# Kernel tuning notes

Hardware: AMD Instinct MI355X
Metric: run time of the kernel (lower is better)

## Reference

```python
import jax, jax.numpy as jnp
import numpy as np

N_NODES = 50000
N_EDGES = 800000
D = 128


def _degrees(idx, n):
    # in/out degree via segment_sum of ones, clamped to >=1 (DGL clamp)
    ones = jnp.ones(idx.shape[0], dtype=jnp.float32)
    return jnp.clip(jax.ops.segment_sum(ones, idx, num_segments=n), 1.0)


def graph_conv(x, src, dst, W, b):
    # DGL GraphConv, norm='both', aggregate-then-matmul (in_feats == out_feats)
    n = x.shape[0]
    deg_out = _degrees(src, n)  # [N]
    deg_in = _degrees(dst, n)   # [N]
    xs = x * jax.lax.rsqrt(deg_out)[:, None]          # [N, D] pre-normalize
    msg = jax.ops.segment_sum(xs[src], dst, num_segments=n)  # gather+scatter [N, D]
    h = msg * jax.lax.rsqrt(deg_in)[:, None]
    return h @ W + b


def setup_inputs() -> dict:
    key = jax.random.key(0)
    k1, k2, k3, k4, k5 = jax.random.split(key, 5)
    x = jax.random.normal(k1, (N_NODES, D), dtype=jnp.float32)
    src = jax.random.randint(k2, (N_EDGES,), 0, N_NODES, dtype=jnp.int64)
    dst = jax.random.randint(k3, (N_EDGES,), 0, N_NODES, dtype=jnp.int64)
    scale = 1.0 / np.sqrt(D)
    W1 = jax.random.normal(k4, (D, D), dtype=jnp.float32) * scale
    W2 = jax.random.normal(k5, (D, D), dtype=jnp.float32) * scale
    b1 = jnp.zeros((D,), dtype=jnp.float32)
    b2 = jnp.zeros((D,), dtype=jnp.float32)
    return {"x": x, "src": src, "dst": dst, "W1": W1, "b1": b1, "W2": W2, "b2": b2}


def reference(x, src, dst, W1, b1, W2, b2):
    h = graph_conv(x, src, dst, W1, b1)
    h = jax.nn.relu(h)
    return graph_conv(h, src, dst, W2, b2)
```

## Files before the change

### kernel.cpp

```cpp
#include <hip/hip_runtime.h>

#define N_NODES 50000
#define N_EDGES 800000
#define D 128
#define CAP 64
#define OVF_CAP 4096

#define HB 160
#define CHUNK ((N_EDGES + HB - 1) / HB)
#define NW (N_NODES / 4)

typedef unsigned short bf16_t;
typedef __attribute__((ext_vector_type(8))) short short8v;
typedef __attribute__((ext_vector_type(4))) float f32x4;

__device__ inline float bf2f(bf16_t u) {
    union { unsigned int i; float f; } v;
    v.i = ((unsigned int)u) << 16;
    return v.f;
}
__device__ inline bf16_t f2bf(float f) {
    union { float f; unsigned int i; } v;
    v.f = f;
    unsigned int u = v.i;
    unsigned int r = (u + 0x7FFFu + ((u >> 16) & 1u)) >> 16;
    return (bf16_t)r;
}
__device__ inline float u2f_lo(unsigned int u) {
    union { unsigned int i; float f; } x; x.i = u << 16; return x.f;
}
__device__ inline float u2f_hi(unsigned int u) {
    union { unsigned int i; float f; } x; x.i = u & 0xFFFF0000u; return x.f;
}


__global__ __launch_bounds__(1024) void hist_kernel(const int* __restrict__ src,
                                                    const int* __restrict__ dst,
                                                    unsigned int* __restrict__ Hs,
                                                    unsigned int* __restrict__ Hd, int nE) {
    __shared__ unsigned int hs[NW];
    __shared__ unsigned int hd[NW];
    for (int i = threadIdx.x; i < NW; i += 1024) { hs[i] = 0u; hd[i] = 0u; }
    __syncthreads();
    int e0 = blockIdx.x * CHUNK;
    int e1 = min(e0 + CHUNK, nE);
    for (int e = e0 + (int)threadIdx.x; e < e1; e += 1024) {
        int s = src[e];
        int d = dst[e];
        atomicAdd(&hs[s >> 2], 1u << (8 * (s & 3)));
        atomicAdd(&hd[d >> 2], 1u << (8 * (d & 3)));
    }
    __syncthreads();
    unsigned int* Hsb = Hs + (size_t)blockIdx.x * NW;
    unsigned int* Hdb = Hd + (size_t)blockIdx.x * NW;
    for (int i = threadIdx.x; i < NW; i += 1024) { Hsb[i] = hs[i]; Hdb[i] = hd[i]; }
}

__global__ void scan_kernel(const unsigned int* __restrict__ Hs,
                            const unsigned int* __restrict__ Hd,
                            unsigned int* __restrict__ OFF,
                            int* __restrict__ cnt_s, int* __restrict__ cnt_d) {
    int w = blockIdx.x * 256 + (int)threadIdx.x;
    if (w >= NW) return;
    if (blockIdx.y == 0) {
        unsigned int run = 0;
        for (int b = 0; b < HB; b++) {
            unsigned int v = Hd[(size_t)b * NW + w];
            OFF[(size_t)b * NW + w] = run;
            run += v;
        }
        int4 c;
        c.x = (int)(run & 0xFFu); c.y = (int)((run >> 8) & 0xFFu);
        c.z = (int)((run >> 16) & 0xFFu); c.w = (int)(run >> 24);
        ((int4*)cnt_d)[w] = c;
    } else {
        unsigned int run = 0;
        for (int b = 0; b < HB; b++) run += Hs[(size_t)b * NW + w];
        int4 c;
        c.x = (int)(run & 0xFFu); c.y = (int)((run >> 8) & 0xFFu);
        c.z = (int)((run >> 16) & 0xFFu); c.w = (int)(run >> 24);
        ((int4*)cnt_s)[w] = c;
    }
}

__global__ __launch_bounds__(1024) void place_kernel(const int* __restrict__ src,
                                                     const int* __restrict__ dst,
                                                     const unsigned int* __restrict__ OFF,
                                                     unsigned short* __restrict__ bucket,
                                                     int* __restrict__ ovf_cnt,
                                                     int2* __restrict__ ovf, int nE) {
    __shared__ unsigned int cur[NW];
    const unsigned int* OFFb = OFF + (size_t)blockIdx.x * NW;
    for (int i = threadIdx.x; i < NW; i += 1024) cur[i] = OFFb[i];
    __syncthreads();
    int e0 = blockIdx.x * CHUNK;
    int e1 = min(e0 + CHUNK, nE);
    for (int e = e0 + (int)threadIdx.x; e < e1; e += 1024) {
        int s = src[e];
        int d = dst[e];
        int sh = 8 * (d & 3);
        unsigned int old = atomicAdd(&cur[d >> 2], 1u << sh);
        unsigned int q = (old >> sh) & 0xFFu;
        if (q < CAP) {
            bucket[(size_t)d * CAP + q] = (unsigned short)s;
        } else {
            int o = atomicAdd(ovf_cnt, 1);
            if (o < OVF_CAP) ovf[o] = make_int2(d, s);
        }
    }
}

__global__ void prescale_kernel(const float4* __restrict__ x, const int* __restrict__ cnt_s,
                                const int* __restrict__ cnt_d,
                                float* __restrict__ rs_out, float* __restrict__ rs_in,
                                ushort4* __restrict__ xs4, int nN) {
    int node = blockIdx.x * 8 + (threadIdx.x >> 5);
    int c = threadIdx.x & 31;
    if (node >= nN) return;
    float rs_o = 0.0f;
    if (c == 0) {
        rs_o = rsqrtf(fmaxf((float)cnt_s[node], 1.0f));
        rs_out[node] = rs_o;
        rs_in[node] = rsqrtf(fmaxf((float)cnt_d[node], 1.0f));
    }
    rs_o = __shfl(rs_o, threadIdx.x & 32);
    float4 v = x[(size_t)node * 32 + c];
    ushort4 o;
    o.x = f2bf(v.x * rs_o);
    o.y = f2bf(v.y * rs_o);
    o.z = f2bf(v.z * rs_o);
    o.w = f2bf(v.w * rs_o);
    xs4[(size_t)node * 32 + c] = o;
}

__global__ void gather_kernel(const uint4* __restrict__ xs,
                              const int* __restrict__ cnt_d,
                              const unsigned short* __restrict__ bucket,
                              float4* __restrict__ msg4, int nN) {
    int node = blockIdx.x * 16 + ((int)threadIdx.x >> 4);
    int lane = threadIdx.x & 15;
    if (node >= nN) return;
    const unsigned short* bk = bucket + (size_t)node * CAP;
    int cnt = min(cnt_d[node], CAP);
    float a[8];
#pragma unroll
    for (int k = 0; k < 8; k++) a[k] = 0.f;
#define ACC8(v)                                              \
    a[0] += u2f_lo(v.x); a[1] += u2f_hi(v.x);                \
    a[2] += u2f_lo(v.y); a[3] += u2f_hi(v.y);                \
    a[4] += u2f_lo(v.z); a[5] += u2f_hi(v.z);                \
    a[6] += u2f_lo(v.w); a[7] += u2f_hi(v.w);
    int e = 0;
    for (; e + 3 < cnt; e += 4) {
        int s0 = bk[e], s1 = bk[e + 1], s2 = bk[e + 2], s3 = bk[e + 3];
        uint4 v0 = xs[(size_t)s0 * 16 + lane];
        uint4 v1 = xs[(size_t)s1 * 16 + lane];
        uint4 v2 = xs[(size_t)s2 * 16 + lane];
        uint4 v3 = xs[(size_t)s3 * 16 + lane];
        ACC8(v0) ACC8(v1) ACC8(v2) ACC8(v3)
    }
    for (; e < cnt; e++) {
        int s0 = bk[e];
        uint4 v0 = xs[(size_t)s0 * 16 + lane];
        ACC8(v0)
    }
#undef ACC8
    size_t o = (size_t)node * 32 + lane * 2;
    msg4[o]     = make_float4(a[0], a[1], a[2], a[3]);
    msg4[o + 1] = make_float4(a[4], a[5], a[6], a[7]);
}

__global__ void ovf_kernel(const int2* __restrict__ ovf, const int* __restrict__ ovf_cnt,
                           const ushort4* __restrict__ xs4, float* __restrict__ msg) {
    int n = min(*ovf_cnt, OVF_CAP);
    int lane = threadIdx.x & 31;
    for (int i = (int)(threadIdx.x >> 5); i < n; i += 8) {
        int2 ds = ovf[i];
        ushort4 v = xs4[(size_t)ds.y * 32 + lane];
        float* m = msg + (size_t)ds.x * D + lane * 4;
        atomicAdd(m + 0, bf2f(v.x));
        atomicAdd(m + 1, bf2f(v.y));
        atomicAdd(m + 2, bf2f(v.z));
        atomicAdd(m + 3, bf2f(v.w));
    }
}

__global__ void wsplit_kernel(const float* __restrict__ W1, bf16_t* __restrict__ Wf1,
                              const float* __restrict__ W2, bf16_t* __restrict__ Wf2) {
    const float* W = blockIdx.y ? W2 : W1;
    bf16_t* Wf = blockIdx.y ? Wf2 : Wf1;
    int flat = blockIdx.x * 256 + (int)threadIdx.x;
    int lane = flat & 63;
    int c = (flat >> 6) & 7;
    int ks = flat >> 9;
    int n = c * 16 + (lane & 15);
    int kb = ks * 32 + (lane >> 4) * 8;
#pragma unroll
    for (int j = 0; j < 8; j++) {
        float w = W[(size_t)(kb + j) * D + n];
        bf16_t hi = f2bf(w);
        bf16_t lo = f2bf(w - bf2f(hi));
        Wf[(size_t)flat * 8 + j] = hi;
        Wf[(size_t)(2048 + flat) * 8 + j] = lo;
    }
}

template <bool RELU_OUTSCALE, bool OUT_BF16>
__global__ __launch_bounds__(256) void gemm_mfma_kernel(
    const float* __restrict__ msg, const float* __restrict__ rs_in,
    const float* __restrict__ rs_out, const bf16_t* __restrict__ Wf,
    const float* __restrict__ bias, void* __restrict__ outp, int nN) {
    int lane = (int)threadIdx.x & 63;
    int wave = (int)threadIdx.x >> 6;
    int n0 = blockIdx.x * 64 + wave * 16;
    int ar = lane & 15;
    int kg = lane >> 4;

    short8v ahi[4], alo[4];
    {
        const float* ap = msg + (size_t)(n0 + ar) * D + kg * 8;
        bool valid = (n0 + ar) < nN;
#pragma unroll
        for (int ks = 0; ks < 4; ks++) {
            float av[8];
            if (valid) {
                float4 p0 = *(const float4*)(ap + ks * 32);
                float4 p1 = *(const float4*)(ap + ks * 32 + 4);
                av[0] = p0.x; av[1] = p0.y; av[2] = p0.z; av[3] = p0.w;
                av[4] = p1.x; av[5] = p1.y; av[6] = p1.z; av[7] = p1.w;
            } else {
#pragma unroll
                for (int j = 0; j < 8; j++) av[j] = 0.f;
            }
#pragma unroll
            for (int j = 0; j < 8; j++) {
                bf16_t h = f2bf(av[j]);
                bf16_t l = f2bf(av[j] - bf2f(h));
                ahi[ks][j] = (short)h;
                alo[ks][j] = (short)l;
            }
        }
    }

    f32x4 acc[8];
#pragma unroll
    for (int c = 0; c < 8; c++) acc[c] = (f32x4){0.f, 0.f, 0.f, 0.f};

    const short8v* Bh = (const short8v*)Wf;
    const short8v* Bl = Bh + 2048;
#pragma unroll
    for (int ks = 0; ks < 4; ks++) {
#pragma unroll
        for (int c = 0; c < 8; c++) {
            int off = (ks * 8 + c) * 64 + lane;
            short8v wh = Bh[off];
            short8v wl = Bl[off];
            acc[c] = __builtin_amdgcn_mfma_f32_16x16x32_bf16(ahi[ks], wh, acc[c], 0, 0, 0);
            acc[c] = __builtin_amdgcn_mfma_f32_16x16x32_bf16(alo[ks], wh, acc[c], 0, 0, 0);
            acc[c] = __builtin_amdgcn_mfma_f32_16x16x32_bf16(ahi[ks], wl, acc[c], 0, 0, 0);
        }
    }

    int ocol = lane & 15;
#pragma unroll
    for (int r = 0; r < 4; r++) {
        int node = n0 + kg * 4 + r;
        if (node >= nN) continue;
        float ri = rs_in[node];
        float ro = RELU_OUTSCALE ? rs_out[node] : 1.0f;
#pragma unroll
        for (int c = 0; c < 8; c++) {
            float v = acc[c][r] * ri + bias[c * 16 + ocol];
            if (RELU_OUTSCALE) v = fmaxf(v, 0.0f) * ro;
            if (OUT_BF16) {
                ((bf16_t*)outp)[(size_t)node * D + c * 16 + ocol] = f2bf(v);
            } else {
                ((float*)outp)[(size_t)node * D + c * 16 + ocol] = v;
            }
        }
    }
}

static inline size_t align16(size_t x) { return (x + 15) & ~(size_t)15; }

extern "C" void kernel_launch(void* const* d_in, const int* in_sizes, int n_in,
                              void* d_out, int out_size, void* d_ws, size_t ws_size,
                              hipStream_t stream) {
    const float* x   = (const float*)d_in[0];
    const int*   src = (const int*)d_in[1];
    const int*   dst = (const int*)d_in[2];
    const float* W1  = (const float*)d_in[3];
    const float* b1  = (const float*)d_in[4];
    const float* W2  = (const float*)d_in[5];
    const float* b2  = (const float*)d_in[6];
    float* out = (float*)d_out;

    char* p = (char*)d_ws;
    float*          msg     = (float*)p;          p += align16((size_t)N_NODES * D * sizeof(float));
    int*            cnt_s   = (int*)p;            p += align16(N_NODES * sizeof(int));
    int*            cnt_d   = (int*)p;            p += align16(N_NODES * sizeof(int));
    int*            ovf_cnt = (int*)p;            p += align16(16 * sizeof(int));
    int2*           ovf     = (int2*)p;           p += align16((size_t)OVF_CAP * sizeof(int2));
    unsigned short* bucket  = (unsigned short*)p; p += align16((size_t)N_NODES * CAP * sizeof(unsigned short));
    float*          rs_out  = (float*)p;          p += align16(N_NODES * sizeof(float));
    float*          rs_in   = (float*)p;          p += align16(N_NODES * sizeof(float));
    bf16_t*         Wf1     = (bf16_t*)p;         p += align16((size_t)2 * 2048 * 8 * sizeof(bf16_t));
    bf16_t*         Wf2     = (bf16_t*)p;         p += align16((size_t)2 * 2048 * 8 * sizeof(bf16_t));
    bf16_t*         xs      = (bf16_t*)p;
    bf16_t*         hs      = xs;

    unsigned int* Hs  = (unsigned int*)msg;
    unsigned int* Hd  = Hs + (size_t)HB * NW;
    unsigned int* OFF = Hd + (size_t)HB * NW;

    hipMemsetAsync(ovf_cnt, 0, 16 * sizeof(int), stream);

    wsplit_kernel<<<dim3(8, 2), 256, 0, stream>>>(W1, Wf1, W2, Wf2);

    hist_kernel<<<HB, 1024, 0, stream>>>(src, dst, Hs, Hd, N_EDGES);
    scan_kernel<<<dim3((NW + 255) / 256, 2), 256, 0, stream>>>(Hs, Hd, OFF, cnt_s, cnt_d);
    place_kernel<<<HB, 1024, 0, stream>>>(src, dst, OFF, bucket, ovf_cnt, ovf, N_EDGES);

    prescale_kernel<<<(N_NODES + 7) / 8, 256, 0, stream>>>((const float4*)x, cnt_s, cnt_d,
                                                           rs_out, rs_in, (ushort4*)xs, N_NODES);

    int ggrid = (N_NODES + 15) / 16;
    int mgrid = (N_NODES + 63) / 64;

    gather_kernel<<<ggrid, 256, 0, stream>>>((const uint4*)xs, cnt_d, bucket,
                                             (float4*)msg, N_NODES);
    ovf_kernel<<<1, 256, 0, stream>>>(ovf, ovf_cnt, (const ushort4*)xs, msg);

    gemm_mfma_kernel<true, true><<<mgrid, 256, 0, stream>>>(
        msg, rs_in, rs_out, Wf1, b1, hs, N_NODES);

    gather_kernel<<<ggrid, 256, 0, stream>>>((const uint4*)hs, cnt_d, bucket,
                                             (float4*)msg, N_NODES);
    ovf_kernel<<<1, 256, 0, stream>>>(ovf, ovf_cnt, (const ushort4*)hs, msg);

    gemm_mfma_kernel<false, false><<<mgrid, 256, 0, stream>>>(
        msg, rs_in, nullptr, Wf2, b2, out, N_NODES);
}
```

Before: 243.0 us.

## Replace histogram/scan/place pipeline with single node-partitioned LDS bucket scatter kernel

Replaces the three-kernel CSR build (per-chunk histograms, a scan over 160 histograms, then placement) with one kernel of 40 blocks. Each block owns 1250 destination nodes, reads the whole edge list, builds its buckets and degree counts in LDS, then writes them to global memory with coalesced stores. This removes the large intermediate histogram and offset traffic and two kernel launches. In exchange every block reads all 800K edges (40x redundant reads), only 40 CUs are used, and the per-node bucket capacity drops from 64 to 48, which may send more edges to the overflow path. Bucket slot order now depends on atomic timing rather than chunk order.

```diff
diff --git a/kernel.cpp b/kernel.cpp
--- a/kernel.cpp
+++ b/kernel.cpp
@@ -3,12 +3,11 @@
 #define N_NODES 50000
 #define N_EDGES 800000
 #define D 128
-#define CAP 64
+#define CAP 48
 #define OVF_CAP 4096
 
-#define HB 160
-#define CHUNK ((N_EDGES + HB - 1) / HB)
-#define NW (N_NODES / 4)
+#define NPART 40
+#define PNODES 1250
 
 typedef unsigned short bf16_t;
 typedef __attribute__((ext_vector_type(8))) short short8v;
@@ -33,80 +32,40 @@
     union { unsigned int i; float f; } x; x.i = u & 0xFFFF0000u; return x.f;
 }
 
-
-__global__ __launch_bounds__(1024) void hist_kernel(const int* __restrict__ src,
-                                                    const int* __restrict__ dst,
-                                                    unsigned int* __restrict__ Hs,
-                                                    unsigned int* __restrict__ Hd, int nE) {
-    __shared__ unsigned int hs[NW];
-    __shared__ unsigned int hd[NW];
-    for (int i = threadIdx.x; i < NW; i += 1024) { hs[i] = 0u; hd[i] = 0u; }
+__global__ __launch_bounds__(1024) void scatter_kernel(
+    const int* __restrict__ src, const int* __restrict__ dst,
+    unsigned short* __restrict__ bucket, int* __restrict__ cnt_s,
+    int* __restrict__ cnt_d, int* __restrict__ ovf_cnt, int2* __restrict__ ovf, int nE) {
+    __shared__ unsigned short bk[PNODES * CAP];
+    __shared__ unsigned int cur[PNODES];
+    __shared__ unsigned int hsrc[PNODES];
+    const int nbeg = blockIdx.x * PNODES;
+    for (int i = threadIdx.x; i < PNODES; i += 1024) { cur[i] = 0u; hsrc[i] = 0u; }
     __syncthreads();
-    int e0 = blockIdx.x * CHUNK;
-    int e1 = min(e0 + CHUNK, nE);
-    for (int e = e0 + (int)threadIdx.x; e < e1; e += 1024) {
+    for (int e = (int)threadIdx.x; e < nE; e += 1024) {
         int s = src[e];
         int d = dst[e];
-        atomicAdd(&hs[s >> 2], 1u << (8 * (s & 3)));
-        atomicAdd(&hd[d >> 2], 1u << (8 * (d & 3)));
+        unsigned ss = (unsigned)(s - nbeg);
+        unsigned dd = (unsigned)(d - nbeg);
+        if (ss < PNODES) atomicAdd(&hsrc[ss], 1u);
+        if (dd < PNODES) {
+            unsigned q = atomicAdd(&cur[dd], 1u);
+            if (q < CAP) {
+                bk[dd * CAP + q] = (unsigned short)s;
+            } else {
+                int o = atomicAdd(ovf_cnt, 1);
+                if (o < OVF_CAP) ovf[o] = make_int2(d, s);
+            }
+        }
     }
     __syncthreads();
-    unsigned int* Hsb = Hs + (size_t)blockIdx.x * NW;
-    unsigned int* Hdb = Hd + (size_t)blockIdx.x * NW;
-    for (int i = threadIdx.x; i < NW; i += 1024) { Hsb[i] = hs[i]; Hdb[i] = hd[i]; }
-}
-
-__global__ void scan_kernel(const unsigned int* __restrict__ Hs,
-                            const unsigned int* __restrict__ Hd,
-                            unsigned int* __restrict__ OFF,
-                            int* __restrict__ cnt_s, int* __restrict__ cnt_d) {
-    int w = blockIdx.x * 256 + (int)threadIdx.x;
-    if (w >= NW) return;
-    if (blockIdx.y == 0) {
-        unsigned int run = 0;
-        for (int b = 0; b < HB; b++) {
-            unsigned int v = Hd[(size_t)b * NW + w];
-            OFF[(size_t)b * NW + w] = run;
-            run += v;
-        }
-        int4 c;
-        c.x = (int)(run & 0xFFu); c.y = (int)((run >> 8) & 0xFFu);
-        c.z = (int)((run >> 16) & 0xFFu); c.w = (int)(run >> 24);
-        ((int4*)cnt_d)[w] = c;
-    } else {
-        unsigned int run = 0;
-        for (int b = 0; b < HB; b++) run += Hs[(size_t)b * NW + w];
-        int4 c;
-        c.x = (int)(run & 0xFFu); c.y = (int)((run >> 8) & 0xFFu);
-        c.z = (int)((run >> 16) & 0xFFu); c.w = (int)(run >> 24);
-        ((int4*)cnt_s)[w] = c;
-    }
-}
-
-__global__ __launch_bounds__(1024) void place_kernel(const int* __restrict__ src,
-                                                     const int* __restrict__ dst,
-                                                     const unsigned int* __restrict__ OFF,
-                                                     unsigned short* __restrict__ bucket,
-                                                     int* __restrict__ ovf_cnt,
-                                                     int2* __restrict__ ovf, int nE) {
-    __shared__ unsigned int cur[NW];
-    const unsigned int* OFFb = OFF + (size_t)blockIdx.x * NW;
-    for (int i = threadIdx.x; i < NW; i += 1024) cur[i] = OFFb[i];
-    __syncthreads();
-    int e0 = blockIdx.x * CHUNK;
-    int e1 = min(e0 + CHUNK, nE);
-    for (int e = e0 + (int)threadIdx.x; e < e1; e += 1024) {
-        int s = src[e];
-        int d = dst[e];
-        int sh = 8 * (d & 3);
-        unsigned int old = atomicAdd(&cur[d >> 2], 1u << sh);
-        unsigned int q = (old >> sh) & 0xFFu;
-        if (q < CAP) {
-            bucket[(size_t)d * CAP + q] = (unsigned short)s;
-        } else {
-            int o = atomicAdd(ovf_cnt, 1);
-            if (o < OVF_CAP) ovf[o] = make_int2(d, s);
-        }
+    uint4* gb = (uint4*)(bucket + (size_t)nbeg * CAP);
+    const uint4* lb = (const uint4*)bk;
+    const int n16 = PNODES * CAP * 2 / 16;
+    for (int i = threadIdx.x; i < n16; i += 1024) gb[i] = lb[i];
+    for (int i = threadIdx.x; i < PNODES; i += 1024) {
+        cnt_d[nbeg + i] = (int)cur[i];
+        cnt_s[nbeg + i] = (int)hsrc[i];
     }
 }
 
@@ -309,17 +268,12 @@
     bf16_t*         xs      = (bf16_t*)p;
     bf16_t*         hs      = xs;
 
-    unsigned int* Hs  = (unsigned int*)msg;
-    unsigned int* Hd  = Hs + (size_t)HB * NW;
-    unsigned int* OFF = Hd + (size_t)HB * NW;
-
     hipMemsetAsync(ovf_cnt, 0, 16 * sizeof(int), stream);
 
     wsplit_kernel<<<dim3(8, 2), 256, 0, stream>>>(W1, Wf1, W2, Wf2);
 
-    hist_kernel<<<HB, 1024, 0, stream>>>(src, dst, Hs, Hd, N_EDGES);
-    scan_kernel<<<dim3((NW + 255) / 256, 2), 256, 0, stream>>>(Hs, Hd, OFF, cnt_s, cnt_d);
-    place_kernel<<<HB, 1024, 0, stream>>>(src, dst, OFF, bucket, ovf_cnt, ovf, N_EDGES);
+    scatter_kernel<<<NPART, 1024, 0, stream>>>(src, dst, bucket, cnt_s, cnt_d,
+                                               ovf_cnt, ovf, N_EDGES);
 
     prescale_kernel<<<(N_NODES + 7) / 8, 256, 0, stream>>>((const float4*)x, cnt_s, cnt_d,
                                                            rs_out, rs_in, (ushort4*)xs, N_NODES);
```

Measured after the change: 515.4 us. 2.12x slower.
